# Performance work log

Hardware: AMD Instinct MI355X
Metric: run time of the kernel (lower is better)

The kernel has to match this reference:

```python
import jax, jax.numpy as jnp
import numpy as np

NUM_EXPERTS = 64
TOP_K = 8
TEMPERATURE = 1.0


def setup_inputs() -> dict:
    key = jax.random.key(0)
    k1, k2 = jax.random.split(key)
    B, D, E = 32768, 2048, NUM_EXPERTS
    r = jax.random.normal(k1, (B, D), dtype=jnp.float32)
    W = jax.random.normal(k2, (E, D), dtype=jnp.float32) * (1.0 / np.sqrt(D))
    b = jnp.zeros((E,), dtype=jnp.float32)
    return {"r": r, "W": W, "b": b}


def reference(r, W, b):
    # logits: (B, E) = r @ W^T + b, then temperature scaling
    logits = (jnp.einsum('bd,ed->be', r, W) + b) / TEMPERATURE
    weights_soft = jax.nn.softmax(logits, axis=-1)
    if TOP_K is not None and TOP_K < NUM_EXPERTS:
        topk_vals, topk_idx = jax.lax.top_k(weights_soft, TOP_K)
        mask = jnp.zeros_like(weights_soft)
        mask = jax.vmap(lambda m, i: m.at[i].set(1.0))(mask, topk_idx)
        weights_hard = weights_soft * mask
        weights_hard = weights_hard / (weights_hard.sum(axis=-1, keepdims=True) + 1e-9)
    else:
        weights_hard = weights_soft
    return (weights_hard, weights_soft)
```

## Files before the change

### kernel.cpp

```cpp
#include <hip/hip_runtime.h>
#include <hip/hip_bf16.h>
#include <stdint.h>


#define D_DIM 2048
#define E_DIM 64
#define B_DIM 32768
#define TOPK 8

typedef __bf16 bf16x8 __attribute__((ext_vector_type(8)));
typedef float f32x4 __attribute__((ext_vector_type(4)));

__global__ __launch_bounds__(256) void w_prep(const float* __restrict__ W,
                                              __bf16* __restrict__ P) {
    const int K = blockIdx.x;
    const int u = threadIdx.x;
    const float* src = W + (size_t)(u >> 2) * D_DIM + K * 32 + (u & 3) * 8;
    __bf16* dst = P + (size_t)K * 6144 + u * 8;
    bf16x8 o1, o2, o3;
    #pragma unroll
    for (int j = 0; j < 8; ++j) {
        float x  = src[j];
        __bf16 h1 = (__bf16)x;
        float r1 = x - (float)h1;
        __bf16 h2 = (__bf16)r1;
        float r2 = r1 - (float)h2;
        o1[j] = h1; o2[j] = h2; o3[j] = (__bf16)r2;
    }
    *(bf16x8*)(dst)        = o1;
    *(bf16x8*)(dst + 2048) = o2;
    *(bf16x8*)(dst + 4096) = o3;
}

__device__ __forceinline__ void gload_lds16(const void* g, void* s) {
    __builtin_amdgcn_global_load_lds(
        (const __attribute__((address_space(1))) unsigned int*)g,
        (__attribute__((address_space(3))) unsigned int*)s,
        16, 0, 0);
}

__global__ __launch_bounds__(512, 4) void moe_gate(const float* __restrict__ r,
                                                   const __bf16* __restrict__ P,
                                                   const float* __restrict__ bias,
                                                   float* __restrict__ out) {
    __shared__ __align__(16) char smem[2 * 2 * 3 * 2048 * 2];

    __bf16 (*bstage)[2][3][2048] = reinterpret_cast<__bf16 (*)[2][3][2048]>(smem);
    float  (*lg)[E_DIM + 1]      = reinterpret_cast<float (*)[E_DIM + 1]>(smem);

    const int t    = threadIdx.x;
    const int wv   = t >> 6;
    const int lane = t & 63;
    const int lrow = lane & 15;
    const int quad = lane >> 4;
    const int h    = wv >> 2;
    const int wq   = wv & 3;
    const int tl   = t & 255;
    const int row0 = blockIdx.x * 64;

    const __bf16* Pb = P + (size_t)h * 32 * 6144 + tl * 8;

    const float* ra = r + (size_t)(row0 + wq * 16 + lrow) * D_DIM + h * 1024 + quad * 8;

    f32x4 accM[4] = {};
    f32x4 accD[4] = {};
    f32x4 accL[4] = {};

    #pragma unroll
    for (int s = 0; s < 3; ++s)
        gload_lds16(Pb + s * 2048, &bstage[h][0][s][tl * 8]);
    float4 a0 = *(const float4*)(ra);
    float4 a1 = *(const float4*)(ra + 4);

    for (int ks = 0; ks < 32; ++ks) {
        __syncthreads();
        const int kn = ks + 1;
        if (kn < 32) {
            #pragma unroll
            for (int s = 0; s < 3; ++s)
                gload_lds16(Pb + (size_t)kn * 6144 + s * 2048,
                            &bstage[h][kn & 1][s][tl * 8]);
        }

        float av[8] = {a0.x, a0.y, a0.z, a0.w, a1.x, a1.y, a1.z, a1.w};
        if (kn < 32) {
            a0 = *(const float4*)(ra + kn * 32);
            a1 = *(const float4*)(ra + kn * 32 + 4);
        }
        bf16x8 A1, A2, A3;
        #pragma unroll
        for (int j = 0; j < 8; ++j) {
            float x  = av[j];
            __bf16 h1 = (__bf16)x;
            float r1 = x - (float)h1;
            __bf16 h2 = (__bf16)r1;
            float r2 = r1 - (float)h2;
            A1[j] = h1; A2[j] = h2; A3[j] = (__bf16)r2;
        }

        const __bf16* bb = &bstage[h][ks & 1][0][0];
        const int fo = quad * 8 + lrow * 32;
        bf16x8 B[3][4];
        #pragma unroll
        for (int s = 0; s < 3; ++s)
            #pragma unroll
            for (int n = 0; n < 4; ++n)
                B[s][n] = *(const bf16x8*)(bb + (size_t)s * 2048 + n * 512 + fo);

        #pragma unroll
        for (int n = 0; n < 4; ++n) {
            accM[n] = __builtin_amdgcn_mfma_f32_16x16x32_bf16(A1, B[0][n], accM[n], 0, 0, 0);
            accD[n] = __builtin_amdgcn_mfma_f32_16x16x32_bf16(A1, B[1][n], accD[n], 0, 0, 0);
            accD[n] = __builtin_amdgcn_mfma_f32_16x16x32_bf16(A2, B[0][n], accD[n], 0, 0, 0);
            accL[n] = __builtin_amdgcn_mfma_f32_16x16x32_bf16(A1, B[2][n], accL[n], 0, 0, 0);
            accL[n] = __builtin_amdgcn_mfma_f32_16x16x32_bf16(A2, B[1][n], accL[n], 0, 0, 0);
            accL[n] = __builtin_amdgcn_mfma_f32_16x16x32_bf16(A3, B[0][n], accL[n], 0, 0, 0);
        }
    }

    __syncthreads();

    if (h == 0) {
        #pragma unroll
        for (int n = 0; n < 4; ++n) {
            int col = n * 16 + lrow;
            #pragma unroll
            for (int i = 0; i < 4; ++i)
                lg[wq * 16 + quad * 4 + i][col] = accM[n][i] + (accD[n][i] + accL[n][i]);
        }
    }
    __syncthreads();
    if (h == 1) {
        #pragma unroll
        for (int n = 0; n < 4; ++n) {
            int col = n * 16 + lrow;
            #pragma unroll
            for (int i = 0; i < 4; ++i)
                lg[wq * 16 + quad * 4 + i][col] += accM[n][i] + (accD[n][i] + accL[n][i]);
        }
    }
    __syncthreads();

    const float bcol = bias[lane];
    for (int rr = wv; rr < 64; rr += 8) {
        float logit = lg[rr][lane] + bcol;
        float mx = logit;
        #pragma unroll
        for (int s = 32; s >= 1; s >>= 1) mx = fmaxf(mx, __shfl_xor(mx, s));
        float ex = expf(logit - mx);
        float sm = ex;
        #pragma unroll
        for (int s = 32; s >= 1; s >>= 1) sm += __shfl_xor(sm, s);
        float soft = ex / sm;

        bool  sel    = false;
        float topsum = 0.0f;
        #pragma unroll
        for (int it = 0; it < TOPK; ++it) {
            float cand = sel ? -1.0f : soft;
            float cm = cand;
            #pragma unroll
            for (int s = 32; s >= 1; s >>= 1) cm = fmaxf(cm, __shfl_xor(cm, s));
            unsigned long long ball = __ballot(cand == cm);
            int leader = __ffsll(ball) - 1;
            if (lane == leader) sel = true;
            topsum += cm;
        }
        float hard = sel ? soft / (topsum + 1e-9f) : 0.0f;

        size_t orow = (size_t)(row0 + rr) * E_DIM + lane;
        out[orow] = hard;
        out[(size_t)B_DIM * E_DIM + orow] = soft;
    }
}

extern "C" void kernel_launch(void* const* d_in, const int* in_sizes, int n_in,
                              void* d_out, int out_size, void* d_ws, size_t ws_size,
                              hipStream_t stream) {
    const float* r = (const float*)d_in[0];
    const float* W = (const float*)d_in[1];
    const float* b = (const float*)d_in[2];
    float* out = (float*)d_out;
    __bf16* P = (__bf16*)d_ws;

    w_prep<<<64, 256, 0, stream>>>(W, P);
    moe_gate<<<512, 512, 0, stream>>>(r, P, b, out);
}
```

Before: 412.3 us.

## Split K across four waves with direct global B loads instead of LDS staging

Each block now covers 16 rows instead of 64, and its four waves each take a quarter of the K dimension. The wave-specific split-bf16 weight fragments are read straight from global memory (likely L2-resident) into registers, replacing the double-buffered LDS staging and the per-iteration barriers. Partial logits from the four waves are summed in shared memory before the softmax and top-k epilogue. This drops the barriers and LDS traffic and launches four times as many blocks, at the cost of B no longer being shared across row tiles in LDS, so L2 and global weight reads go up fourfold.

```diff
diff --git a/kernel.cpp b/kernel.cpp
--- a/kernel.cpp
+++ b/kernel.cpp
@@ -7,6 +7,7 @@
 #define E_DIM 64
 #define B_DIM 32768
 #define TOPK 8
+#define NK 16
 
 typedef __bf16 bf16x8 __attribute__((ext_vector_type(8)));
 typedef float f32x4 __attribute__((ext_vector_type(4)));
@@ -32,61 +33,47 @@
     *(bf16x8*)(dst + 4096) = o3;
 }
 
-__device__ __forceinline__ void gload_lds16(const void* g, void* s) {
-    __builtin_amdgcn_global_load_lds(
-        (const __attribute__((address_space(1))) unsigned int*)g,
-        (__attribute__((address_space(3))) unsigned int*)s,
-        16, 0, 0);
-}
-
-__global__ __launch_bounds__(512, 4) void moe_gate(const float* __restrict__ r,
+__global__ __launch_bounds__(256, 4) void moe_gate(const float* __restrict__ r,
                                                    const __bf16* __restrict__ P,
                                                    const float* __restrict__ bias,
                                                    float* __restrict__ out) {
-    __shared__ __align__(16) char smem[2 * 2 * 3 * 2048 * 2];
-
-    __bf16 (*bstage)[2][3][2048] = reinterpret_cast<__bf16 (*)[2][3][2048]>(smem);
-    float  (*lg)[E_DIM + 1]      = reinterpret_cast<float (*)[E_DIM + 1]>(smem);
+    __shared__ float lg[4][16][E_DIM + 1];
 
     const int t    = threadIdx.x;
     const int wv   = t >> 6;
     const int lane = t & 63;
     const int lrow = lane & 15;
     const int quad = lane >> 4;
-    const int h    = wv >> 2;
-    const int wq   = wv & 3;
-    const int tl   = t & 255;
-    const int row0 = blockIdx.x * 64;
+    const int row0 = blockIdx.x * 16;
 
-    const __bf16* Pb = P + (size_t)h * 32 * 6144 + tl * 8;
-
-    const float* ra = r + (size_t)(row0 + wq * 16 + lrow) * D_DIM + h * 1024 + quad * 8;
+    const __bf16* Pq = P + (size_t)wv * NK * 6144 + quad * 8 + lrow * 32;
+    const float* ra = r + (size_t)(row0 + lrow) * D_DIM + wv * 512 + quad * 8;
 
     f32x4 accM[4] = {};
     f32x4 accD[4] = {};
     f32x4 accL[4] = {};
 
-    #pragma unroll
-    for (int s = 0; s < 3; ++s)
-        gload_lds16(Pb + s * 2048, &bstage[h][0][s][tl * 8]);
     float4 a0 = *(const float4*)(ra);
     float4 a1 = *(const float4*)(ra + 4);
 
-    for (int ks = 0; ks < 32; ++ks) {
-        __syncthreads();
+    #pragma unroll 2
+    for (int ks = 0; ks < NK; ++ks) {
         const int kn = ks + 1;
-        if (kn < 32) {
-            #pragma unroll
-            for (int s = 0; s < 3; ++s)
-                gload_lds16(Pb + (size_t)kn * 6144 + s * 2048,
-                            &bstage[h][kn & 1][s][tl * 8]);
+        float4 na0 = a0, na1 = a1;
+        if (kn < NK) {
+            na0 = *(const float4*)(ra + kn * 32);
+            na1 = *(const float4*)(ra + kn * 32 + 4);
         }
 
+        const __bf16* bb = Pq + (size_t)ks * 6144;
+        bf16x8 B[3][4];
+        #pragma unroll
+        for (int s = 0; s < 3; ++s)
+            #pragma unroll
+            for (int n = 0; n < 4; ++n)
+                B[s][n] = *(const bf16x8*)(bb + s * 2048 + n * 512);
+
         float av[8] = {a0.x, a0.y, a0.z, a0.w, a1.x, a1.y, a1.z, a1.w};
-        if (kn < 32) {
-            a0 = *(const float4*)(ra + kn * 32);
-            a1 = *(const float4*)(ra + kn * 32 + 4);
-        }
         bf16x8 A1, A2, A3;
         #pragma unroll
         for (int j = 0; j < 8; ++j) {
@@ -98,15 +85,6 @@
             A1[j] = h1; A2[j] = h2; A3[j] = (__bf16)r2;
         }
 
-        const __bf16* bb = &bstage[h][ks & 1][0][0];
-        const int fo = quad * 8 + lrow * 32;
-        bf16x8 B[3][4];
-        #pragma unroll
-        for (int s = 0; s < 3; ++s)
-            #pragma unroll
-            for (int n = 0; n < 4; ++n)
-                B[s][n] = *(const bf16x8*)(bb + (size_t)s * 2048 + n * 512 + fo);
-
         #pragma unroll
         for (int n = 0; n < 4; ++n) {
             accM[n] = __builtin_amdgcn_mfma_f32_16x16x32_bf16(A1, B[0][n], accM[n], 0, 0, 0);
@@ -116,34 +94,23 @@
             accL[n] = __builtin_amdgcn_mfma_f32_16x16x32_bf16(A2, B[1][n], accL[n], 0, 0, 0);
             accL[n] = __builtin_amdgcn_mfma_f32_16x16x32_bf16(A3, B[0][n], accL[n], 0, 0, 0);
         }
+
+        a0 = na0; a1 = na1;
     }
 
-    __syncthreads();
-
-    if (h == 0) {
+    #pragma unroll
+    for (int n = 0; n < 4; ++n) {
+        int col = n * 16 + lrow;
         #pragma unroll
-        for (int n = 0; n < 4; ++n) {
-            int col = n * 16 + lrow;
-            #pragma unroll
-            for (int i = 0; i < 4; ++i)
-                lg[wq * 16 + quad * 4 + i][col] = accM[n][i] + (accD[n][i] + accL[n][i]);
-        }
-    }
-    __syncthreads();
-    if (h == 1) {
-        #pragma unroll
-        for (int n = 0; n < 4; ++n) {
-            int col = n * 16 + lrow;
-            #pragma unroll
-            for (int i = 0; i < 4; ++i)
-                lg[wq * 16 + quad * 4 + i][col] += accM[n][i] + (accD[n][i] + accL[n][i]);
-        }
+        for (int i = 0; i < 4; ++i)
+            lg[wv][quad * 4 + i][col] = accM[n][i] + (accD[n][i] + accL[n][i]);
     }
     __syncthreads();
 
     const float bcol = bias[lane];
-    for (int rr = wv; rr < 64; rr += 8) {
-        float logit = lg[rr][lane] + bcol;
+    for (int rr = wv; rr < 16; rr += 4) {
+        float logit = ((lg[0][rr][lane] + lg[1][rr][lane]) +
+                       (lg[2][rr][lane] + lg[3][rr][lane])) + bcol;
         float mx = logit;
         #pragma unroll
         for (int s = 32; s >= 1; s >>= 1) mx = fmaxf(mx, __shfl_xor(mx, s));
@@ -184,5 +151,5 @@
     __bf16* P = (__bf16*)d_ws;
 
     w_prep<<<64, 256, 0, stream>>>(W, P);
-    moe_gate<<<512, 512, 0, stream>>>(r, P, b, out);
+    moe_gate<<<2048, 256, 0, stream>>>(r, P, b, out);
 }
```

After: 442.4 us. 7.3% more time.
